# Kernel tuning notes

Measured on AMD Instinct MI355X. Metric: run time of the kernel, lower is better.

Reference implementation:

```python
import jax, jax.numpy as jnp
import numpy as np

DIM = 512
DIM_HEAD = 64
HEADS = 8
INNER = DIM_HEAD * HEADS  # 512
OUT_DIM = DIM
PB_ALPHA = 128.0
EPS = 1e-5
SCALE = DIM_HEAD ** (-0.5) / PB_ALPHA


def layer_norm(x, g):
    mean = jnp.mean(x, axis=-1, keepdims=True)
    var = jnp.mean(jnp.square(x - mean), axis=-1, keepdims=True)  # unbiased=False
    return (x - mean) * jax.lax.rsqrt(var + EPS) * g


def setup_inputs() -> dict:
    key = jax.random.key(0)
    ks = jax.random.split(key, 6)
    b, n, r = 4, 64, 256
    x = jax.random.normal(ks[0], (b, n, r, DIM), dtype=jnp.float32)
    g_norm = jnp.ones((DIM,), dtype=jnp.float32)
    W_q = jax.random.normal(ks[1], (DIM, INNER), dtype=jnp.float32) * (DIM ** -0.5)
    W_kv = jax.random.normal(ks[2], (DIM, 2 * DIM_HEAD), dtype=jnp.float32) * (DIM ** -0.5)
    W_out = jax.random.normal(ks[3], (INNER, OUT_DIM), dtype=jnp.float32) * (INNER ** -0.5)
    g_out = jnp.ones((OUT_DIM,), dtype=jnp.float32)
    return {"x": x, "g_norm": g_norm, "W_q": W_q, "W_kv": W_kv, "W_out": W_out, "g_out": g_out}


def reference(x, g_norm, W_q, W_kv, W_out, g_out):
    b, n, r, _ = x.shape
    xn = layer_norm(x, g_norm)                      # [b,n,r,dim]
    q = xn @ W_q                                    # [b,n,r,h*d]
    kv = xn @ W_kv                                  # context defaults to x
    k, v = jnp.split(kv, 2, axis=-1)                # [b,n,r,d] each, shared over heads
    q = q.reshape(b, n, r, HEADS, DIM_HEAD).transpose(0, 1, 3, 2, 4)  # b n h i d
    q = q * SCALE
    sim = jnp.einsum('bnhid,bnjd->bnhij', q, k)
    sim = (sim - jax.lax.stop_gradient(jnp.max(sim, axis=-1, keepdims=True))) * PB_ALPHA
    attn = jax.nn.softmax(sim, axis=-1)
    out = jnp.einsum('bnhij,bnjd->bnhid', attn, v)  # b n h i d
    out = out.transpose(0, 1, 3, 2, 4).reshape(b, n, r, INNER)  # b n i (h d)
    out = out @ W_out
    return layer_norm(out, g_out)
```

## Files before the change

### kernel.cpp

```cpp
#include <hip/hip_runtime.h>
#include <stdint.h>


#define DIM   512
#define DHEAD 64
#define RLEN  256
#define TOK   65536
#define NALL  640

typedef __bf16 bf16;
typedef __bf16 bf16x4 __attribute__((ext_vector_type(4)));
typedef __bf16 bf16x8 __attribute__((ext_vector_type(8)));
typedef float  f32x4  __attribute__((ext_vector_type(4)));
typedef short  s16x4  __attribute__((ext_vector_type(4)));

__device__ __forceinline__ f32x4 mfma16(bf16x8 a, bf16x8 b, f32x4 c) {
  return __builtin_amdgcn_mfma_f32_16x16x32_bf16(a, b, c, 0, 0, 0);
}
__device__ __forceinline__ f32x4 mfma_k16(bf16x4 a, bf16x4 b, f32x4 c) {
#if __has_builtin(__builtin_amdgcn_mfma_f32_16x16x16bf16_1k)
  return __builtin_amdgcn_mfma_f32_16x16x16bf16_1k(
      __builtin_bit_cast(s16x4, a), __builtin_bit_cast(s16x4, b), c, 0, 0, 0);
#else
  f32x4 d = c;
  asm volatile("v_mfma_f32_16x16x16_bf16 %0, %1, %2, %0"
               : "+v"(d) : "v"(a), "v"(b));
  return d;
#endif
}
__device__ __forceinline__ f32x4 fzero4() {
  f32x4 z; z[0] = z[1] = z[2] = z[3] = 0.f; return z;
}
__device__ __forceinline__ void gload_lds16(const void* g, void* l) {
  __builtin_amdgcn_global_load_lds(
      (const __attribute__((address_space(1))) void*)g,
      (__attribute__((address_space(3))) void*)l, 16, 0, 0);
}

__global__ __launch_bounds__(256) void k_prep(
    const float* __restrict__ Wq, const float* __restrict__ Wkv,
    const float* __restrict__ Wout,
    bf16* __restrict__ wall, bf16* __restrict__ woutt) {
  int t = blockIdx.x * 256 + threadIdx.x;
  int n = t >> 9, k = t & 511;
  float v = (n < DIM) ? Wq[k * DIM + n] : Wkv[k * 128 + (n - DIM)];
  wall[t] = (bf16)v;
  if (t < DIM * DIM) woutt[t] = (bf16)Wout[k * DIM + n];
}

__global__ __launch_bounds__(256) void kx_ln(
    const float* __restrict__ x, const float* __restrict__ gnorm,
    bf16* __restrict__ xn) {
  const int lane = threadIdx.x & 63;
  const int gw = blockIdx.x * 4 + (threadIdx.x >> 6);
  float gv[8];
  #pragma unroll
  for (int j = 0; j < 8; ++j) gv[j] = gnorm[lane * 8 + j];
  #pragma unroll
  for (int i = 0; i < 8; ++i) {
    size_t row = (size_t)gw * 8 + i;
    const float4* xp = (const float4*)(x + row * DIM + lane * 8);
    float4 v0 = xp[0], v1 = xp[1];
    float s  = v0.x + v0.y + v0.z + v0.w + v1.x + v1.y + v1.z + v1.w;
    float sq = v0.x*v0.x + v0.y*v0.y + v0.z*v0.z + v0.w*v0.w
             + v1.x*v1.x + v1.y*v1.y + v1.z*v1.z + v1.w*v1.w;
    #pragma unroll
    for (int d = 1; d < 64; d <<= 1) { s += __shfl_xor(s, d); sq += __shfl_xor(sq, d); }
    float mean = s * (1.f / 512.f);
    float var  = sq * (1.f / 512.f) - mean * mean;
    float rs   = rsqrtf(var + 1e-5f);
    bf16x8 o;
    o[0] = (bf16)((v0.x - mean) * rs * gv[0]);
    o[1] = (bf16)((v0.y - mean) * rs * gv[1]);
    o[2] = (bf16)((v0.z - mean) * rs * gv[2]);
    o[3] = (bf16)((v0.w - mean) * rs * gv[3]);
    o[4] = (bf16)((v1.x - mean) * rs * gv[4]);
    o[5] = (bf16)((v1.y - mean) * rs * gv[5]);
    o[6] = (bf16)((v1.z - mean) * rs * gv[6]);
    o[7] = (bf16)((v1.w - mean) * rs * gv[7]);
    *(bf16x8*)(xn + row * DIM + lane * 8) = o;
  }
}

__global__ __launch_bounds__(256) void k_gemm_qkv(
    const bf16* __restrict__ xn, const bf16* __restrict__ wall,
    bf16* __restrict__ qbuf, bf16* __restrict__ kbuf, bf16* __restrict__ vtbuf) {
  __shared__ bf16 sa[2][128 * 32];
  __shared__ bf16 sb[2][128 * 32];
  const int t = threadIdx.x, wave = t >> 6, lane = t & 63;
  const int l15 = lane & 15, g = lane >> 4;
  const int wm = wave >> 1, wn = wave & 1;
  int wg = (blockIdx.x & 7) * 320 + (blockIdx.x >> 3);
  const int bm = wg / 5, bn = wg % 5;
  const char* Abase = (const char*)(xn   + (size_t)bm * 128 * DIM);
  const char* Bbase = (const char*)(wall + (size_t)bn * 128 * DIM);
  const int srow0 = wave * 16 + (lane >> 2);
  const int skb   = (lane & 3) * 16;

  #pragma unroll
  for (int c = 0; c < 2; ++c) {
    int row = c * 64 + srow0;
    int kb = skb ^ ((row & 3) << 4);
    gload_lds16(Abase + (size_t)row * 1024 + kb, (char*)&sa[0][0] + c * 4096 + wave * 1024);
    gload_lds16(Bbase + (size_t)row * 1024 + kb, (char*)&sb[0][0] + c * 4096 + wave * 1024);
  }
  __syncthreads();

  f32x4 acc[4][4];
  #pragma unroll
  for (int mi = 0; mi < 4; ++mi)
    #pragma unroll
    for (int ni = 0; ni < 4; ++ni) acc[mi][ni] = fzero4();

  #pragma unroll 2
  for (int step = 0; step < 16; ++step) {
    const int cur = step & 1;
    if (step < 15) {
      int kk2 = (step + 1) * 64;
      #pragma unroll
      for (int c = 0; c < 2; ++c) {
        int row = c * 64 + srow0;
        int kb = skb ^ ((row & 3) << 4);
        gload_lds16(Abase + (size_t)row * 1024 + kk2 + kb,
                    (char*)&sa[cur ^ 1][0] + c * 4096 + wave * 1024);
        gload_lds16(Bbase + (size_t)row * 1024 + kk2 + kb,
                    (char*)&sb[cur ^ 1][0] + c * 4096 + wave * 1024);
      }
    }
    bf16x8 a[4], b[4];
    #pragma unroll
    for (int mi = 0; mi < 4; ++mi) {
      int row = wm * 64 + mi * 16 + l15;
      a[mi] = *(const bf16x8*)((const char*)&sa[cur][0] + row * 64 + ((g * 16) ^ ((row & 3) << 4)));
    }
    #pragma unroll
    for (int ni = 0; ni < 4; ++ni) {
      int row = wn * 64 + ni * 16 + l15;
      b[ni] = *(const bf16x8*)((const char*)&sb[cur][0] + row * 64 + ((g * 16) ^ ((row & 3) << 4)));
    }
    #pragma unroll
    for (int mi = 0; mi < 4; ++mi)
      #pragma unroll
      for (int ni = 0; ni < 4; ++ni)
        acc[mi][ni] = mfma16(a[mi], b[ni], acc[mi][ni]);
    __syncthreads();
  }

  #pragma unroll
  for (int ni = 0; ni < 4; ++ni) {
    int col0 = bn * 128 + wn * 64 + ni * 16;
    if (col0 < 512) {
      bf16* dst = qbuf + col0 + l15;
      #pragma unroll
      for (int mi = 0; mi < 4; ++mi)
        #pragma unroll
        for (int jj = 0; jj < 4; ++jj) {
          size_t row = (size_t)bm * 128 + wm * 64 + mi * 16 + g * 4 + jj;
          dst[row * DIM] = (bf16)acc[mi][ni][jj];
        }
    } else if (col0 < 576) {
      bf16* dst = kbuf + (col0 - 512) + l15;
      #pragma unroll
      for (int mi = 0; mi < 4; ++mi)
        #pragma unroll
        for (int jj = 0; jj < 4; ++jj) {
          size_t row = (size_t)bm * 128 + wm * 64 + mi * 16 + g * 4 + jj;
          dst[row * DHEAD] = (bf16)acc[mi][ni][jj];
        }
    } else {
      int d = col0 - 576 + l15;
      #pragma unroll
      for (int mi = 0; mi < 4; ++mi) {
        size_t row = (size_t)bm * 128 + wm * 64 + mi * 16 + g * 4;
        int bnr = (int)(row >> 8), kv = (int)(row & 255);
        bf16x4 v4;
        v4[0] = (bf16)acc[mi][ni][0]; v4[1] = (bf16)acc[mi][ni][1];
        v4[2] = (bf16)acc[mi][ni][2]; v4[3] = (bf16)acc[mi][ni][3];
        *(bf16x4*)(vtbuf + (size_t)bnr * 16384 + (size_t)d * 256 + kv) = v4;
      }
    }
  }
}

__global__ __launch_bounds__(512) void k_out_fused(
    const bf16* __restrict__ abuf, const bf16* __restrict__ woutt,
    const float* __restrict__ gout, float* __restrict__ out) {
  __shared__ bf16 sa[2][64 * 32];
  __shared__ bf16 sb[2][512 * 32];
  __shared__ float2 part[64][4];
  __shared__ float2 stats[64];
  const int t = threadIdx.x, wave = t >> 6, lane = t & 63;
  const int l15 = lane & 15, g = lane >> 4;
  const int wm = wave >> 2, wn = wave & 3;
  int wg = (blockIdx.x & 7) * 128 + (blockIdx.x >> 3);
  const size_t row0 = (size_t)wg * 64;
  const char* Abase = (const char*)(abuf + row0 * DIM);
  const int nsub = wave * 16 + (lane >> 2);
  const int skb  = (lane & 3) * 16;

  #pragma unroll
  for (int c = 0; c < 4; ++c) {
    int row = c * 128 + nsub;
    int kb = skb ^ ((row & 3) << 4);
    gload_lds16((const char*)(woutt + (size_t)row * DIM) + kb,
                (char*)&sb[0][0] + c * 8192 + wave * 1024);
  }
  if (t < 256) {
    int kb = skb ^ ((nsub & 3) << 4);
    gload_lds16(Abase + (size_t)nsub * 1024 + kb,
                (char*)&sa[0][0] + wave * 1024 + (lane & 63) * 16);
  }
  __syncthreads();

  f32x4 acc[2][8];
  #pragma unroll
  for (int mi = 0; mi < 2; ++mi)
    #pragma unroll
    for (int ni = 0; ni < 8; ++ni) acc[mi][ni] = fzero4();

  #pragma unroll 2
  for (int step = 0; step < 16; ++step) {
    const int cur = step & 1;
    if (step < 15) {
      int kk2 = (step + 1) * 64;
      #pragma unroll
      for (int c = 0; c < 4; ++c) {
        int row = c * 128 + nsub;
        int kb = skb ^ ((row & 3) << 4);
        gload_lds16((const char*)(woutt + (size_t)row * DIM) + kk2 + kb,
                    (char*)&sb[cur ^ 1][0] + c * 8192 + wave * 1024);
      }
      if (t < 256) {
        int kb = skb ^ ((nsub & 3) << 4);
        gload_lds16(Abase + (size_t)nsub * 1024 + kk2 + kb,
                    (char*)&sa[cur ^ 1][0] + wave * 1024 + lane * 16);
      }
    }
    bf16x8 a[2];
    #pragma unroll
    for (int mi = 0; mi < 2; ++mi) {
      int row = wm * 32 + mi * 16 + l15;
      a[mi] = *(const bf16x8*)((const char*)&sa[cur][0] + row * 64 + ((g * 16) ^ ((row & 3) << 4)));
    }
    #pragma unroll
    for (int ni = 0; ni < 8; ++ni) {
      int row = wn * 128 + ni * 16 + l15;
      bf16x8 b = *(const bf16x8*)((const char*)&sb[cur][0] + row * 64 + ((g * 16) ^ ((row & 3) << 4)));
      acc[0][ni] = mfma16(a[0], b, acc[0][ni]);
      acc[1][ni] = mfma16(a[1], b, acc[1][ni]);
    }
    __syncthreads();
  }

  #pragma unroll
  for (int mi = 0; mi < 2; ++mi)
    #pragma unroll
    for (int jj = 0; jj < 4; ++jj) {
      float s = 0.f, q = 0.f;
      #pragma unroll
      for (int ni = 0; ni < 8; ++ni) {
        float v = acc[mi][ni][jj];
        s += v; q += v * v;
      }
      s += __shfl_xor(s, 1); q += __shfl_xor(q, 1);
      s += __shfl_xor(s, 2); q += __shfl_xor(q, 2);
      s += __shfl_xor(s, 4); q += __shfl_xor(q, 4);
      s += __shfl_xor(s, 8); q += __shfl_xor(q, 8);
      if (l15 == 0) part[wm * 32 + mi * 16 + g * 4 + jj][wn] = make_float2(s, q);
    }
  __syncthreads();
  if (t < 64) {
    float S = 0.f, Q = 0.f;
    #pragma unroll
    for (int w = 0; w < 4; ++w) { S += part[t][w].x; Q += part[t][w].y; }
    float mean = S * (1.f / 512.f);
    float var  = Q * (1.f / 512.f) - mean * mean;
    stats[t] = make_float2(mean, rsqrtf(var + 1e-5f));
  }
  __syncthreads();

  #pragma unroll
  for (int mi = 0; mi < 2; ++mi)
    #pragma unroll
    for (int ni = 0; ni < 8; ++ni) {
      int col = wn * 128 + ni * 16 + l15;
      float gg = gout[col];
      #pragma unroll
      for (int jj = 0; jj < 4; ++jj) {
        int row = wm * 32 + mi * 16 + g * 4 + jj;
        float2 st = stats[row];
        out[(row0 + row) * DIM + col] = (acc[mi][ni][jj] - st.x) * st.y * gg;
      }
    }
}

__global__ __launch_bounds__(512, 2) void k_attn(
    bf16* __restrict__ qbuf, const bf16* __restrict__ kbuf,
    const bf16* __restrict__ vtbuf) {
  __shared__ char lds[256 * 144 + 64 * 528];
  char* lk  = lds;
  char* lvt = lds + 256 * 144;
  const int t = threadIdx.x, lane = t & 63;
  const int l15 = lane & 15, g = lane >> 4;
  int wg = (blockIdx.x & 7) * 256 + (blockIdx.x >> 3);
  const int bn = wg >> 3, h = wg & 7;
  const size_t tok0 = (size_t)bn * RLEN;
  const int m0 = (t >> 6) * 32;

  bf16x8 aq[2][2];
  {
    const bf16* qb = qbuf + (tok0 + m0 + l15) * DIM + h * DHEAD + g * 8;
    #pragma unroll
    for (int qh = 0; qh < 2; ++qh)
      #pragma unroll
      for (int ks = 0; ks < 2; ++ks)
        aq[qh][ks] = *(const bf16x8*)(qb + (size_t)qh * 16 * DIM + ks * 32);
  }
  {
    const bf16* ksrc = kbuf + tok0 * DHEAD;
    const bf16* vsrc = vtbuf + (size_t)bn * (64 * 256);
    bf16x8 kr[4], vr[4];
    #pragma unroll
    for (int i = 0; i < 4; ++i) kr[i] = *(const bf16x8*)(ksrc + (i * 512 + t) * 8);
    #pragma unroll
    for (int i = 0; i < 4; ++i) vr[i] = *(const bf16x8*)(vsrc + (i * 512 + t) * 8);
    #pragma unroll
    for (int i = 0; i < 4; ++i) {
      int off = i * 512 + t;
      *(bf16x8*)(lk + (off >> 3) * 144 + (off & 7) * 16) = kr[i];
    }
    #pragma unroll
    for (int i = 0; i < 4; ++i) {
      int off = i * 512 + t;
      *(bf16x8*)(lvt + (off >> 5) * 528 + (off & 31) * 16) = vr[i];
    }
  }
  __syncthreads();

  const char* bk_base = lk  + l15 * 144 + g * 16;
  const char* bv_base = lvt + l15 * 528 + g * 8;

  const float C = 0.1803368801f;
  f32x4 o2[2][4];
  #pragma unroll
  for (int qh = 0; qh < 2; ++qh)
    #pragma unroll
    for (int di = 0; di < 4; ++di) o2[qh][di] = fzero4();
  float lsum0 = 0.f, lsum1 = 0.f;

  __builtin_amdgcn_s_setprio(1);
  #pragma unroll
  for (int f = 0; f < 16; ++f) {
    bf16x8 bk0 = *(const bf16x8*)(bk_base + f * 2304);
    bf16x8 bk1 = *(const bf16x8*)(bk_base + f * 2304 + 64);
    f32x4 s0 = mfma16(bk0, aq[0][0], fzero4());
    s0 = mfma16(bk1, aq[0][1], s0);
    f32x4 s1 = mfma16(bk0, aq[1][0], fzero4());
    s1 = mfma16(bk1, aq[1][1], s1);
    float p00 = exp2f(s0[0] * C), p01 = exp2f(s0[1] * C);
    float p02 = exp2f(s0[2] * C), p03 = exp2f(s0[3] * C);
    float p10 = exp2f(s1[0] * C), p11 = exp2f(s1[1] * C);
    float p12 = exp2f(s1[2] * C), p13 = exp2f(s1[3] * C);
    lsum0 += (p00 + p01) + (p02 + p03);
    lsum1 += (p10 + p11) + (p12 + p13);
    bf16x4 pk0, pk1;
    pk0[0] = (bf16)p00; pk0[1] = (bf16)p01; pk0[2] = (bf16)p02; pk0[3] = (bf16)p03;
    pk1[0] = (bf16)p10; pk1[1] = (bf16)p11; pk1[2] = (bf16)p12; pk1[3] = (bf16)p13;
    #pragma unroll
    for (int di = 0; di < 4; ++di) {
      bf16x4 bv = *(const bf16x4*)(bv_base + di * 8448 + f * 32);
      o2[0][di] = mfma_k16(pk0, bv, o2[0][di]);
      o2[1][di] = mfma_k16(pk1, bv, o2[1][di]);
    }
  }
  __builtin_amdgcn_s_setprio(0);

  float linv[2];
  lsum0 += __shfl_xor(lsum0, 16); lsum0 += __shfl_xor(lsum0, 32);
  lsum1 += __shfl_xor(lsum1, 16); lsum1 += __shfl_xor(lsum1, 32);
  linv[0] = 1.0f / lsum0;
  linv[1] = 1.0f / lsum1;

  #pragma unroll
  for (int qh = 0; qh < 2; ++qh)
    #pragma unroll
    for (int jj = 0; jj < 4; ++jj) {
      float inv = __shfl(linv[qh], 4 * g + jj);
      size_t row = tok0 + m0 + qh * 16 + 4 * g + jj;
      #pragma unroll
      for (int di = 0; di < 4; ++di)
        qbuf[row * DIM + h * DHEAD + di * 16 + l15] = (bf16)(o2[qh][di][jj] * inv);
    }
}

extern "C" void kernel_launch(void* const* d_in, const int* in_sizes, int n_in,
                              void* d_out, int out_size, void* d_ws, size_t ws_size,
                              hipStream_t stream) {
  const float* x     = (const float*)d_in[0];
  const float* gnorm = (const float*)d_in[1];
  const float* Wq    = (const float*)d_in[2];
  const float* Wkv   = (const float*)d_in[3];
  const float* Wout  = (const float*)d_in[4];
  const float* gout  = (const float*)d_in[5];
  float* out = (float*)d_out;
  char* ws = (char*)d_ws;
  bf16* wall  = (bf16*)(ws);
  bf16* woutt = (bf16*)(ws + 655360);
  bf16* xnbuf = (bf16*)(ws + 1179648);
  bf16* qbuf  = (bf16*)(ws + 1179648 + (size_t)TOK * DIM * 2);
  bf16* kbuf  = (bf16*)((char*)qbuf + (size_t)TOK * DIM * 2);
  bf16* vtbuf = (bf16*)((char*)kbuf + (size_t)TOK * DHEAD * 2);

  k_prep     <<<dim3(1280), dim3(256), 0, stream>>>(Wq, Wkv, Wout, wall, woutt);
  kx_ln      <<<dim3(2048), dim3(256), 0, stream>>>(x, gnorm, xnbuf);
  k_gemm_qkv <<<dim3(2560), dim3(256), 0, stream>>>(xnbuf, wall, qbuf, kbuf, vtbuf);
  k_attn     <<<dim3(2048), dim3(512), 0, stream>>>(qbuf, kbuf, vtbuf);
  k_out_fused<<<dim3(1024), dim3(512), 0, stream>>>(qbuf, woutt, gout, out);
}
```

Before: 242.9 us.

## Split QKV GEMM into large-tile Q GEMM and separate KV GEMM

```diff
diff --git a/kernel.cpp b/kernel.cpp
--- a/kernel.cpp
+++ b/kernel.cpp
@@ -6,7 +6,6 @@
 #define DHEAD 64
 #define RLEN  256
 #define TOK   65536
-#define NALL  640
 
 typedef __bf16 bf16;
 typedef __bf16 bf16x4 __attribute__((ext_vector_type(4)));
@@ -82,18 +81,111 @@
   }
 }
 
-__global__ __launch_bounds__(256) void k_gemm_qkv(
+__global__ __launch_bounds__(512) void k_gemm_q(
     const bf16* __restrict__ xn, const bf16* __restrict__ wall,
-    bf16* __restrict__ qbuf, bf16* __restrict__ kbuf, bf16* __restrict__ vtbuf) {
+    bf16* __restrict__ qbuf) {
+  __shared__ bf16 sa[2][256 * 64];
+  __shared__ bf16 sb[2][256 * 64];
+  const int t = threadIdx.x, wave = t >> 6, lane = t & 63;
+  const int l15 = lane & 15, g = lane >> 4;
+  const int wm = wave >> 2, wn = wave & 3;
+  int wg = (blockIdx.x & 7) * 64 + (blockIdx.x >> 3);
+  const int bm = wg >> 1, bn = wg & 1;
+  const char* Abase = (const char*)(xn   + (size_t)bm * 256 * DIM);
+  const char* Bbase = (const char*)(wall + (size_t)bn * 256 * DIM);
+
+  #pragma unroll
+  for (int i = 0; i < 4; ++i) {
+    int chunk = i * 512 + t;
+    int row = chunk >> 3, unit = chunk & 7;
+    int so = row * 1024 + ((unit ^ (row & 7)) << 4);
+    gload_lds16(Abase + so, (char*)&sa[0][0] + i * 8192 + wave * 1024);
+    gload_lds16(Bbase + so, (char*)&sb[0][0] + i * 8192 + wave * 1024);
+  }
+  f32x4 acc[8][4];
+  #pragma unroll
+  for (int mi = 0; mi < 8; ++mi)
+    #pragma unroll
+    for (int ni = 0; ni < 4; ++ni) acc[mi][ni] = fzero4();
+  __syncthreads();
+
+  for (int tt = 0; tt < 8; ++tt) {
+    const int cur = tt & 1;
+    const char* sac = (const char*)&sa[cur][0];
+    const char* sbc = (const char*)&sb[cur][0];
+    char* san = (char*)&sa[cur ^ 1][0];
+    char* sbn = (char*)&sb[cur ^ 1][0];
+    bf16x8 bfr[4];
+    #pragma unroll
+    for (int p = 0; p < 4; ++p) {
+      const int ks = p >> 1, half = p & 1;
+      bf16x8 afr[4];
+      #pragma unroll
+      for (int q = 0; q < 4; ++q) {
+        int row = wm * 128 + half * 64 + q * 16 + l15;
+        int unit = (ks * 4 + g) ^ (row & 7);
+        afr[q] = *(const bf16x8*)(sac + row * 128 + unit * 16);
+      }
+      if (half == 0) {
+        #pragma unroll
+        for (int q = 0; q < 4; ++q) {
+          int row = wn * 64 + q * 16 + l15;
+          int unit = (ks * 4 + g) ^ (row & 7);
+          bfr[q] = *(const bf16x8*)(sbc + row * 128 + unit * 16);
+        }
+      }
+      if (tt < 7 && p < 2) {
+        #pragma unroll
+        for (int i = p * 2; i < p * 2 + 2; ++i) {
+          int chunk = i * 512 + t;
+          int row = chunk >> 3, unit = chunk & 7;
+          int so = row * 1024 + (tt + 1) * 128 + ((unit ^ (row & 7)) << 4);
+          gload_lds16(Abase + so, san + i * 8192 + wave * 1024);
+          gload_lds16(Bbase + so, sbn + i * 8192 + wave * 1024);
+        }
+      }
+      asm volatile("s_barrier" ::: "memory");
+      __builtin_amdgcn_s_setprio(1);
+      #pragma unroll
+      for (int q = 0; q < 4; ++q)
+        #pragma unroll
+        for (int ni = 0; ni < 4; ++ni)
+          acc[half * 4 + q][ni] = mfma16(afr[q], bfr[ni], acc[half * 4 + q][ni]);
+      __builtin_amdgcn_s_setprio(0);
+      if (p == 3) {
+        asm volatile("s_waitcnt vmcnt(0)" ::: "memory");
+      }
+      asm volatile("s_barrier" ::: "memory");
+    }
+  }
+
+  const float QSC = 0.1803368801f;
+  #pragma unroll
+  for (int ni = 0; ni < 4; ++ni) {
+    int col = bn * 256 + wn * 64 + ni * 16 + l15;
+    bf16* dst = qbuf + col;
+    #pragma unroll
+    for (int mi = 0; mi < 8; ++mi)
+      #pragma unroll
+      for (int jj = 0; jj < 4; ++jj) {
+        size_t row = (size_t)bm * 256 + wm * 128 + mi * 16 + g * 4 + jj;
+        dst[row * DIM] = (bf16)(acc[mi][ni][jj] * QSC);
+      }
+  }
+}
+
+__global__ __launch_bounds__(256) void k_gemm_kv(
+    const bf16* __restrict__ xn, const bf16* __restrict__ wkv,
+    bf16* __restrict__ kbuf, bf16* __restrict__ vtbuf) {
   __shared__ bf16 sa[2][128 * 32];
   __shared__ bf16 sb[2][128 * 32];
   const int t = threadIdx.x, wave = t >> 6, lane = t & 63;
   const int l15 = lane & 15, g = lane >> 4;
   const int wm = wave >> 1, wn = wave & 1;
-  int wg = (blockIdx.x & 7) * 320 + (blockIdx.x >> 3);
-  const int bm = wg / 5, bn = wg % 5;
-  const char* Abase = (const char*)(xn   + (size_t)bm * 128 * DIM);
-  const char* Bbase = (const char*)(wall + (size_t)bn * 128 * DIM);
+  int wg = (blockIdx.x & 7) * 64 + (blockIdx.x >> 3);
+  const int bm = wg;
+  const char* Abase = (const char*)(xn + (size_t)bm * 128 * DIM);
+  const char* Bbase = (const char*)wkv;
   const int srow0 = wave * 16 + (lane >> 2);
   const int skb   = (lane & 3) * 16;
 
@@ -148,18 +240,9 @@
 
   #pragma unroll
   for (int ni = 0; ni < 4; ++ni) {
-    int col0 = bn * 128 + wn * 64 + ni * 16;
-    if (col0 < 512) {
-      bf16* dst = qbuf + col0 + l15;
-      #pragma unroll
-      for (int mi = 0; mi < 4; ++mi)
-        #pragma unroll
-        for (int jj = 0; jj < 4; ++jj) {
-          size_t row = (size_t)bm * 128 + wm * 64 + mi * 16 + g * 4 + jj;
-          dst[row * DIM] = (bf16)acc[mi][ni][jj];
-        }
-    } else if (col0 < 576) {
-      bf16* dst = kbuf + (col0 - 512) + l15;
+    int col0 = wn * 64 + ni * 16;
+    if (col0 < 64) {
+      bf16* dst = kbuf + col0 + l15;
       #pragma unroll
       for (int mi = 0; mi < 4; ++mi)
         #pragma unroll
@@ -168,7 +251,7 @@
           dst[row * DHEAD] = (bf16)acc[mi][ni][jj];
         }
     } else {
-      int d = col0 - 576 + l15;
+      int d = col0 - 64 + l15;
       #pragma unroll
       for (int mi = 0; mi < 4; ++mi) {
         size_t row = (size_t)bm * 128 + wm * 64 + mi * 16 + g * 4;
@@ -340,7 +423,6 @@
   const char* bk_base = lk  + l15 * 144 + g * 16;
   const char* bv_base = lvt + l15 * 528 + g * 8;
 
-  const float C = 0.1803368801f;
   f32x4 o2[2][4];
   #pragma unroll
   for (int qh = 0; qh < 2; ++qh)
@@ -357,10 +439,10 @@
     s0 = mfma16(bk1, aq[0][1], s0);
     f32x4 s1 = mfma16(bk0, aq[1][0], fzero4());
     s1 = mfma16(bk1, aq[1][1], s1);
-    float p00 = exp2f(s0[0] * C), p01 = exp2f(s0[1] * C);
-    float p02 = exp2f(s0[2] * C), p03 = exp2f(s0[3] * C);
-    float p10 = exp2f(s1[0] * C), p11 = exp2f(s1[1] * C);
-    float p12 = exp2f(s1[2] * C), p13 = exp2f(s1[3] * C);
+    float p00 = exp2f(s0[0]), p01 = exp2f(s0[1]);
+    float p02 = exp2f(s0[2]), p03 = exp2f(s0[3]);
+    float p10 = exp2f(s1[0]), p11 = exp2f(s1[1]);
+    float p12 = exp2f(s1[2]), p13 = exp2f(s1[3]);
     lsum0 += (p00 + p01) + (p02 + p03);
     lsum1 += (p10 + p11) + (p12 + p13);
     bf16x4 pk0, pk1;
@@ -413,7 +495,8 @@
 
   k_prep     <<<dim3(1280), dim3(256), 0, stream>>>(Wq, Wkv, Wout, wall, woutt);
   kx_ln      <<<dim3(2048), dim3(256), 0, stream>>>(x, gnorm, xnbuf);
-  k_gemm_qkv <<<dim3(2560), dim3(256), 0, stream>>>(xnbuf, wall, qbuf, kbuf, vtbuf);
+  k_gemm_q   <<<dim3(512),  dim3(512), 0, stream>>>(xnbuf, wall, qbuf);
+  k_gemm_kv  <<<dim3(512),  dim3(256), 0, stream>>>(xnbuf, wall + (size_t)512 * DIM, kbuf, vtbuf);
   k_attn     <<<dim3(2048), dim3(512), 0, stream>>>(qbuf, kbuf, vtbuf);
   k_out_fused<<<dim3(1024), dim3(512), 0, stream>>>(qbuf, woutt, gout, out);
 }
```

After: 253.4 us. +4.3%, slower.
